# Optimization experiments

Measured on AMD Instinct MI355X. Metric: run time of the kernel, lower is better.

The kernel has to match this reference:

```python
import jax, jax.numpy as jnp
import numpy as np

# Module hyperparameters (from init_kwargs)
C = 128        # in_channel
L = 16         # seq_len
K = 7          # filter_size
DIL = 1        # dilation
G = 4          # num_groups
SPAN = (K - 1) * DIL + 1
PAD = (SPAN - 1) // 2

B, H, W = 8, 56, 56


def setup_inputs() -> dict:
    key = jax.random.key(0)
    k1, k2 = jax.random.split(key)
    x = jax.random.normal(k1, (B, C, L, H, W), dtype=jnp.float32)
    # kaiming_normal(mode='fan_out', nonlinearity='relu'):
    # fan_out = shape[0] * K * K, std = sqrt(2 / fan_out)
    std = (2.0 / (C * K * K)) ** 0.5
    filter_weight = jax.random.normal(k2, (C, L, K, K), dtype=jnp.float32) * std
    return {"x": x, "filter_weight": filter_weight}


def reference(x, filter_weight):
    # x: (B, C, T, H, W) ; filter_weight: (C, T, K, K)
    b, c, t, h, w = x.shape
    # zero-pad spatial dims
    x2 = jnp.pad(x, ((0, 0), (0, 0), (0, 0), (PAD, PAD), (PAD, PAD)))
    # x1: temporally shifted input (frame t-1, first frame duplicated)
    x1 = jnp.concatenate([x[:, :, :1], x[:, :, :-1]], axis=2)

    outs = []
    # static K*K offset loop (dy slow, dx fast -> matches torch meshgrid 'ij' flatten order)
    for dy in range(0, SPAN, DIL):
        for dx in range(0, SPAN, DIL):
            w_ct = filter_weight[:, :, dy // DIL, dx // DIL]  # (C, T)
            shifted = jax.lax.slice(
                x2, (0, 0, 0, dy, dx), (b, c, t, dy + h, dx + w))
            prod = w_ct[None, :, :, None, None] * x1 * shifted  # (B,C,T,H,W)
            # groupwise channel mean -> (B, G, T, H, W)
            resp = prod.reshape(b, G, c // G, t, h, w).mean(axis=2)
            outs.append(resp)
    # concat over offsets along channel dim -> (B, K^2*G, T, H, W)
    return jnp.concatenate(outs, axis=1)
```

## Files before the change

### kernel.cpp

```cpp
#include <hip/hip_runtime.h>
#include <cstdint>

#define C_ 128
#define L_ 16
#define G_ 4
#define H_ 56
#define W_ 56
#define HW_ 3136
#define CH_ 2
#define NCK_ 16
#define NR_ 5
#define WBUF_F (CH_ * NR_ * 64)
#define WL_F 2048
#define LDS_F (WL_F + 4 * 2 * WBUF_F)
#define XT_ (CH_ * NR_ * 16)

typedef float f4 __attribute__((ext_vector_type(4)));
typedef __attribute__((address_space(3))) uint32_t lds_u32;
typedef const __attribute__((address_space(1))) uint32_t glb_u32;

__global__ __launch_bounds__(256, 2)
void wcorr(const float* __restrict__ x, const float* __restrict__ wgt,
           float* __restrict__ out) {
  __shared__ float lds[LDS_F];

  int bid = blockIdx.x;
  int wid = (bid & 7) * 896 + (bid >> 3);
  int htile = wid % 14;
  int rest = wid / 14;
  int t = rest & 15;
  int bg = rest >> 4;
  int g = bg & 3;
  int b = bg >> 2;
  int h0 = htile * 4;

  int tid = threadIdx.x;
  int lane = tid & 63;
  int wvu = __builtin_amdgcn_readfirstlane(tid >> 6);
  int tx = tid & 7;
  int slot = tid >> 3;
  int h = slot & 3;
  int dy = slot >> 2;
  bool active = (dy < 7) && (tx < 7);
  int dyc = dy < 7 ? dy : 6;
  int txc = tx < 7 ? tx : 6;
  int r = h + dyc;
  int lr = r - 2 * wvu;
  int t1 = t > 0 ? t - 1 : 0;
  int w0 = 8 * txc;

  for (int i = WL_F + tid; i < LDS_F; i += 256) lds[i] = 0.0f;

  {
    const float sc = 1.0f / 32.0f;
    const float* wsrc = wgt + (size_t)(g * 32) * (L_ * 49) + t * 49;
    #pragma unroll
    for (int j = 0; j < 8; ++j) {
      int idx = tid + j * 256;
      int c = idx >> 6;
      int rem = idx & 63;
      int dyy = rem >> 3, dxx = rem & 7;
      float v = 0.0f;
      if (dyy < 7 && dxx < 7)
        v = wsrc[(size_t)c * (L_ * 49) + dyy * 7 + dxx] * sc;
      lds[idx] = v;
    }
  }

  const size_t cstride = (size_t)L_ * HW_;
  const float* xg = x + ((size_t)b * C_ + (size_t)g * 32) * cstride;
  const float* x1b = xg + (size_t)t1 * HW_ + (size_t)(h0 + h) * W_ + w0;

  auto stage = [&](int call, int kb, int c0) {
    int tau = lane + call * 64;
    int row = tau >> 4;
    int sb = tau & 15;
    int ci = (row >= NR_) ? 1 : 0;
    int lrr = row - ci * NR_;
    int rg = 2 * wvu + lrr;
    int vb = sb ^ (rg & 7);
    int hh = h0 - 3 + rg;
    bool ok = (tau < XT_) && (vb >= 1) && (vb <= 14) && (rg <= 9)
              && (hh >= 0) && (hh < H_);
    const float* src = xg + (size_t)(c0 + ci) * cstride + (size_t)t * HW_
                          + hh * W_ + (vb * 4 - 4);
    float* dst = &lds[WL_F + (wvu * 2 + kb) * WBUF_F + call * 256];
    if (ok)
      __builtin_amdgcn_global_load_lds((glb_u32*)src, (lds_u32*)dst, 16, 0, 0);
  };

  float acc[7][8];
  #pragma unroll
  for (int i = 0; i < 7; ++i)
    #pragma unroll
    for (int p = 0; p < 8; ++p) acc[i][p] = 0.0f;

  __syncthreads();

  stage(0, 0, 0); stage(1, 0, 0); stage(2, 0, 0);

  int s = r & 7;
  #pragma unroll 1
  for (int k = 0; k < NCK_; ++k) {
    __builtin_amdgcn_sched_barrier(0);
    int c0 = k * CH_;
    int kb = k & 1;
    const float* x1p0 = x1b + (size_t)(c0 + 0) * cstride;
    const float* x1p1 = x1b + (size_t)(c0 + 1) * cstride;
    f4 a00 = *(const f4*)(x1p0);
    f4 a01 = *(const f4*)(x1p0 + 4);
    f4 a10 = *(const f4*)(x1p1);
    f4 a11 = *(const f4*)(x1p1 + 4);
    if (k + 1 < NCK_) {
      stage(0, kb ^ 1, c0 + CH_);
      stage(1, kb ^ 1, c0 + CH_);
      stage(2, kb ^ 1, c0 + CH_);
      asm volatile("s_waitcnt vmcnt(6)");
    } else {
      asm volatile("s_waitcnt vmcnt(4)");
    }
    __builtin_amdgcn_sched_barrier(0);

    const float* base = &lds[WL_F + (wvu * 2 + kb) * WBUF_F];
    #pragma unroll
    for (int ci = 0; ci < CH_; ++ci) {
      const f4* xsrow = (const f4*)(base + (ci * NR_ + lr) * 64);
      f4 q0 = xsrow[(2 * txc + 0) ^ s];
      f4 q1 = xsrow[(2 * txc + 1) ^ s];
      f4 q2 = xsrow[(2 * txc + 2) ^ s];
      f4 q3 = xsrow[(2 * txc + 3) ^ s];
      const f4* wl = (const f4*)&lds[(c0 + ci) * 64 + dyc * 8];
      f4 wv0 = wl[0];
      f4 wv1 = wl[1];
      f4 a0 = ci ? a10 : a00;
      f4 a1 = ci ? a11 : a01;
      float w7[7] = {wv0.x, wv0.y, wv0.z, wv0.w, wv1.x, wv1.y, wv1.z};
      float rr_[16] = {q0.x, q0.y, q0.z, q0.w, q1.x, q1.y, q1.z, q1.w,
                       q2.x, q2.y, q2.z, q2.w, q3.x, q3.y, q3.z, q3.w};
      float x1v[8] = {a0.x, a0.y, a0.z, a0.w, a1.x, a1.y, a1.z, a1.w};
      #pragma unroll
      for (int dxx = 0; dxx < 7; ++dxx) {
        #pragma unroll
        for (int p = 0; p < 8; ++p) {
          acc[dxx][p] = fmaf(w7[dxx], x1v[p] * rr_[p + dxx + 1], acc[dxx][p]);
        }
      }
    }
  }

  if (active) {
    #pragma unroll
    for (int dxx = 0; dxx < 7; ++dxx) {
      int och = (dy * 7 + dxx) * G_ + g;
      float* op = out + (((size_t)b * 196 + och) * L_ + t) * (size_t)HW_
                      + (size_t)(h0 + h) * W_ + w0;
      f4 o0 = {acc[dxx][0], acc[dxx][1], acc[dxx][2], acc[dxx][3]};
      f4 o1 = {acc[dxx][4], acc[dxx][5], acc[dxx][6], acc[dxx][7]};
      __builtin_nontemporal_store(o0, (f4*)op);
      __builtin_nontemporal_store(o1, (f4*)(op + 4));
    }
  }
}

extern "C" void kernel_launch(void* const* d_in, const int* in_sizes, int n_in,
                              void* d_out, int out_size, void* d_ws, size_t ws_size,
                              hipStream_t stream) {
  const float* x = (const float*)d_in[0];
  const float* w = (const float*)d_in[1];
  float* o = (float*)d_out;
  dim3 grid(7168), block(256);
  hipLaunchKernelGGL(wcorr, grid, block, 0, stream, x, w, o);
}
```

Baseline: 220.4 us.

## Load zero-padding from a zeroed workspace and reorder LDS reads before prefetch

Out-of-bounds stage loads now copy from a zeroed workspace buffer instead of being skipped. This drops the LDS zero-fill loop and the per-iteration predicate and address recomputation, since pointers are now incremented. All LDS operand reads for a chunk are issued before the next chunk's async global-to-LDS prefetch, and the FMA block runs under raised wave priority. It adds a memset launch, a WBUF change to 768 floats, and relies on vmcnt accounting staying correct with the new ordering.

```diff
diff --git a/kernel.cpp b/kernel.cpp
--- a/kernel.cpp
+++ b/kernel.cpp
@@ -10,10 +10,9 @@
 #define CH_ 2
 #define NCK_ 16
 #define NR_ 5
-#define WBUF_F (CH_ * NR_ * 64)
+#define WBUF_F 768
 #define WL_F 2048
 #define LDS_F (WL_F + 4 * 2 * WBUF_F)
-#define XT_ (CH_ * NR_ * 16)
 
 typedef float f4 __attribute__((ext_vector_type(4)));
 typedef __attribute__((address_space(3))) uint32_t lds_u32;
@@ -21,7 +20,7 @@
 
 __global__ __launch_bounds__(256, 2)
 void wcorr(const float* __restrict__ x, const float* __restrict__ wgt,
-           float* __restrict__ out) {
+           float* __restrict__ out, const float* __restrict__ zsrc) {
   __shared__ float lds[LDS_F];
 
   int bid = blockIdx.x;
@@ -49,7 +48,37 @@
   int t1 = t > 0 ? t - 1 : 0;
   int w0 = 8 * txc;
 
-  for (int i = WL_F + tid; i < LDS_F; i += 256) lds[i] = 0.0f;
+  const size_t cstride = (size_t)L_ * HW_;
+  const float* xg = x + ((size_t)b * C_ + (size_t)g * 32) * cstride;
+
+  auto mkstage = [&](int j, const float*& sp, ptrdiff_t& inc) {
+    int tau = lane + j * 64;
+    int row = tau >> 4;
+    int ci = (row >= NR_) ? 1 : 0;
+    int lrr = row - ci * NR_;
+    int rg = 2 * wvu + lrr;
+    int vb = (tau & 15) ^ (rg & 7);
+    int hh = h0 - 3 + rg;
+    bool ok = (row < 2 * NR_) && (vb >= 1) && (vb <= 14)
+              && (hh >= 0) && (hh < H_);
+    sp = ok ? (xg + (size_t)ci * cstride + (size_t)t * HW_
+                  + hh * W_ + (vb * 4 - 4))
+            : (zsrc + (lane & 15) * 4);
+    inc = ok ? (ptrdiff_t)(CH_ * cstride) : 0;
+  };
+  const float *sp0, *sp1, *sp2;
+  ptrdiff_t in0, in1, in2;
+  mkstage(0, sp0, in0);
+  mkstage(1, sp1, in1);
+  mkstage(2, sp2, in2);
+
+  {
+    float* db = &lds[WL_F + (wvu * 2) * WBUF_F];
+    __builtin_amdgcn_global_load_lds((glb_u32*)sp0, (lds_u32*)(db + 0), 16, 0, 0);
+    __builtin_amdgcn_global_load_lds((glb_u32*)sp1, (lds_u32*)(db + 256), 16, 0, 0);
+    __builtin_amdgcn_global_load_lds((glb_u32*)sp2, (lds_u32*)(db + 512), 16, 0, 0);
+    sp0 += in0; sp1 += in1; sp2 += in2;
+  }
 
   {
     const float sc = 1.0f / 32.0f;
@@ -67,27 +96,8 @@
     }
   }
 
-  const size_t cstride = (size_t)L_ * HW_;
-  const float* xg = x + ((size_t)b * C_ + (size_t)g * 32) * cstride;
-  const float* x1b = xg + (size_t)t1 * HW_ + (size_t)(h0 + h) * W_ + w0;
-
-  auto stage = [&](int call, int kb, int c0) {
-    int tau = lane + call * 64;
-    int row = tau >> 4;
-    int sb = tau & 15;
-    int ci = (row >= NR_) ? 1 : 0;
-    int lrr = row - ci * NR_;
-    int rg = 2 * wvu + lrr;
-    int vb = sb ^ (rg & 7);
-    int hh = h0 - 3 + rg;
-    bool ok = (tau < XT_) && (vb >= 1) && (vb <= 14) && (rg <= 9)
-              && (hh >= 0) && (hh < H_);
-    const float* src = xg + (size_t)(c0 + ci) * cstride + (size_t)t * HW_
-                          + hh * W_ + (vb * 4 - 4);
-    float* dst = &lds[WL_F + (wvu * 2 + kb) * WBUF_F + call * 256];
-    if (ok)
-      __builtin_amdgcn_global_load_lds((glb_u32*)src, (lds_u32*)dst, 16, 0, 0);
-  };
+  const float* x1c0 = xg + (size_t)t1 * HW_ + (size_t)(h0 + h) * W_ + w0;
+  const float* x1c1 = x1c0 + cstride;
 
   float acc[7][8];
   #pragma unroll
@@ -97,47 +107,57 @@
 
   __syncthreads();
 
-  stage(0, 0, 0); stage(1, 0, 0); stage(2, 0, 0);
-
   int s = r & 7;
   #pragma unroll 1
   for (int k = 0; k < NCK_; ++k) {
+    int kb = k & 1;
+    int c0 = k * CH_;
+    f4 a00 = *(const f4*)(x1c0);
+    f4 a01 = *(const f4*)(x1c0 + 4);
+    f4 a10 = *(const f4*)(x1c1);
+    f4 a11 = *(const f4*)(x1c1 + 4);
+    x1c0 += CH_ * cstride;
+    x1c1 += CH_ * cstride;
+
     __builtin_amdgcn_sched_barrier(0);
-    int c0 = k * CH_;
-    int kb = k & 1;
-    const float* x1p0 = x1b + (size_t)(c0 + 0) * cstride;
-    const float* x1p1 = x1b + (size_t)(c0 + 1) * cstride;
-    f4 a00 = *(const f4*)(x1p0);
-    f4 a01 = *(const f4*)(x1p0 + 4);
-    f4 a10 = *(const f4*)(x1p1);
-    f4 a11 = *(const f4*)(x1p1 + 4);
-    if (k + 1 < NCK_) {
-      stage(0, kb ^ 1, c0 + CH_);
-      stage(1, kb ^ 1, c0 + CH_);
-      stage(2, kb ^ 1, c0 + CH_);
-      asm volatile("s_waitcnt vmcnt(6)");
-    } else {
-      asm volatile("s_waitcnt vmcnt(4)");
-    }
+    asm volatile("s_waitcnt vmcnt(4)" ::: "memory");
     __builtin_amdgcn_sched_barrier(0);
 
     const float* base = &lds[WL_F + (wvu * 2 + kb) * WBUF_F];
+    const f4* xsrow0 = (const f4*)(base + lr * 64);
+    const f4* xsrow1 = (const f4*)(base + (NR_ + lr) * 64);
+    f4 q00 = xsrow0[(2 * txc + 0) ^ s];
+    f4 q01 = xsrow0[(2 * txc + 1) ^ s];
+    f4 q02 = xsrow0[(2 * txc + 2) ^ s];
+    f4 q03 = xsrow0[(2 * txc + 3) ^ s];
+    f4 q10 = xsrow1[(2 * txc + 0) ^ s];
+    f4 q11 = xsrow1[(2 * txc + 1) ^ s];
+    f4 q12 = xsrow1[(2 * txc + 2) ^ s];
+    f4 q13 = xsrow1[(2 * txc + 3) ^ s];
+    const f4* wl0 = (const f4*)&lds[(c0 + 0) * 64 + dyc * 8];
+    const f4* wl1 = (const f4*)&lds[(c0 + 1) * 64 + dyc * 8];
+    f4 wa0 = wl0[0], wa1 = wl0[1];
+    f4 wb0 = wl1[0], wb1 = wl1[1];
+
+    if (k + 1 < NCK_) {
+      float* db = &lds[WL_F + (wvu * 2 + (kb ^ 1)) * WBUF_F];
+      __builtin_amdgcn_global_load_lds((glb_u32*)sp0, (lds_u32*)(db + 0), 16, 0, 0);
+      __builtin_amdgcn_global_load_lds((glb_u32*)sp1, (lds_u32*)(db + 256), 16, 0, 0);
+      __builtin_amdgcn_global_load_lds((glb_u32*)sp2, (lds_u32*)(db + 512), 16, 0, 0);
+      sp0 += in0; sp1 += in1; sp2 += in2;
+    }
+
+    __builtin_amdgcn_s_setprio(1);
     #pragma unroll
     for (int ci = 0; ci < CH_; ++ci) {
-      const f4* xsrow = (const f4*)(base + (ci * NR_ + lr) * 64);
-      f4 q0 = xsrow[(2 * txc + 0) ^ s];
-      f4 q1 = xsrow[(2 * txc + 1) ^ s];
-      f4 q2 = xsrow[(2 * txc + 2) ^ s];
-      f4 q3 = xsrow[(2 * txc + 3) ^ s];
-      const f4* wl = (const f4*)&lds[(c0 + ci) * 64 + dyc * 8];
-      f4 wv0 = wl[0];
-      f4 wv1 = wl[1];
-      f4 a0 = ci ? a10 : a00;
-      f4 a1 = ci ? a11 : a01;
-      float w7[7] = {wv0.x, wv0.y, wv0.z, wv0.w, wv1.x, wv1.y, wv1.z};
-      float rr_[16] = {q0.x, q0.y, q0.z, q0.w, q1.x, q1.y, q1.z, q1.w,
-                       q2.x, q2.y, q2.z, q2.w, q3.x, q3.y, q3.z, q3.w};
-      float x1v[8] = {a0.x, a0.y, a0.z, a0.w, a1.x, a1.y, a1.z, a1.w};
+      f4 Q0 = ci ? q10 : q00, Q1 = ci ? q11 : q01;
+      f4 Q2 = ci ? q12 : q02, Q3 = ci ? q13 : q03;
+      f4 W0 = ci ? wb0 : wa0, W1 = ci ? wb1 : wa1;
+      f4 A0 = ci ? a10 : a00, A1 = ci ? a11 : a01;
+      float w7[7] = {W0.x, W0.y, W0.z, W0.w, W1.x, W1.y, W1.z};
+      float rr_[16] = {Q0.x, Q0.y, Q0.z, Q0.w, Q1.x, Q1.y, Q1.z, Q1.w,
+                       Q2.x, Q2.y, Q2.z, Q2.w, Q3.x, Q3.y, Q3.z, Q3.w};
+      float x1v[8] = {A0.x, A0.y, A0.z, A0.w, A1.x, A1.y, A1.z, A1.w};
       #pragma unroll
       for (int dxx = 0; dxx < 7; ++dxx) {
         #pragma unroll
@@ -146,6 +166,7 @@
         }
       }
     }
+    __builtin_amdgcn_s_setprio(0);
   }
 
   if (active) {
@@ -168,6 +189,7 @@
   const float* x = (const float*)d_in[0];
   const float* w = (const float*)d_in[1];
   float* o = (float*)d_out;
+  hipMemsetAsync(d_ws, 0, 256, stream);
   dim3 grid(7168), block(256);
-  hipLaunchKernelGGL(wcorr, grid, block, 0, stream, x, w, o);
+  hipLaunchKernelGGL(wcorr, grid, block, 0, stream, x, w, o, (const float*)d_ws);
 }
```

New measurement: 220.0 us. About the same (-0.2%).
